# Performance work log

Measured on AMD Instinct MI355X. Metric: run time of the kernel, lower is better.

The kernel has to match this reference:

```python
import jax, jax.numpy as jnp
import numpy as np

N = 100000   # nodes
E = 300000   # directed edges
D = 256      # emb_dim
G = 4000     # graphs
L = 5        # num_layer
F_IN = 40    # num_atom_features
NUM_BOND_TYPE = 6       # pretrain-gnns convention; self-loop bond type = 4
NUM_BOND_DIRECTION = 3
EPS = 1e-5


def setup_inputs() -> dict:
    key = jax.random.key(0)
    ks = jax.random.split(key, 32)
    s = 0.05
    inp = {}
    inp["x"] = jax.random.normal(ks[0], (N, F_IN), jnp.float32)
    inp["edge_index"] = jax.random.randint(ks[1], (2, E), 0, N)
    inp["edge_attr"] = jax.random.randint(ks[2], (E, 2), 0, 3)
    inp["batch"] = jnp.sort(jax.random.randint(ks[3], (N,), 0, G))
    # atom embedding (Linear + ReLU)
    inp["embW"] = jax.random.normal(ks[4], (F_IN, D), jnp.float32) * s
    inp["embB"] = jnp.zeros((D,), jnp.float32)
    # per-layer GINConv params (stacked over layers)
    inp["ee1"] = jax.random.normal(ks[5], (L, NUM_BOND_TYPE, D), jnp.float32) * s
    inp["ee2"] = jax.random.normal(ks[6], (L, NUM_BOND_DIRECTION, D), jnp.float32) * s
    inp["W1"] = jax.random.normal(ks[7], (L, D, 2 * D), jnp.float32) * s
    inp["b1"] = jnp.zeros((L, 2 * D), jnp.float32)
    inp["W2"] = jax.random.normal(ks[8], (L, 2 * D, D), jnp.float32) * s
    inp["b2"] = jnp.zeros((L, D), jnp.float32)
    inp["bn_g"] = jnp.ones((L, D), jnp.float32)
    inp["bn_b"] = jnp.zeros((L, D), jnp.float32)
    # MLP head: 256 -> 256 -> 128 -> 64 -> 32 -> 1
    dims = [D, D, D // 2, D // 4, D // 8]
    kk = jax.random.split(ks[9], 5)
    for i in range(4):
        inp[f"hW{i}"] = jax.random.normal(kk[i], (dims[i], dims[i + 1]), jnp.float32) * s
        inp[f"hb{i}"] = jnp.zeros((dims[i + 1],), jnp.float32)
    inp["hWo"] = jax.random.normal(kk[4], (dims[4], 1), jnp.float32) * s
    inp["hbo"] = jnp.zeros((1,), jnp.float32)
    return inp


def reference(x, edge_index, edge_attr, batch, embW, embB, ee1, ee2, W1, b1, W2, b2,
              bn_g, bn_b, hW0, hb0, hW1, hb1, hW2, hb2, hW3, hb3, hWo, hbo):
    src, dst = edge_index[0], edge_index[1]
    ea0, ea1 = edge_attr[:, 0], edge_attr[:, 1]
    # x_embedding1: Linear + ReLU
    h = jax.nn.relu(x @ embW + embB)
    for l in range(L):
        # GINConv: gather source features + edge embeddings, scatter-add to dst
        msg = h[src] + ee1[l][ea0] + ee2[l][ea1]        # [E, D]
        agg = jax.ops.segment_sum(msg, dst, num_segments=N)
        # self-loop message (bond type 4, direction 0)
        agg = agg + h + ee1[l][4] + ee2[l][0]
        # GIN MLP: Linear(D, 2D) -> ReLU -> Linear(2D, D)
        h2 = jax.nn.relu(agg @ W1[l] + b1[l]) @ W2[l] + b2[l]
        # BatchNorm1d (training-mode batch statistics, biased variance)
        mu = h2.mean(axis=0)
        var = h2.var(axis=0)
        h2 = (h2 - mu) * jax.lax.rsqrt(var + EPS) * bn_g[l] + bn_b[l]
        if l < L - 1:
            h2 = jax.nn.relu(h2)
        # dropout with drop_ratio=0.0 -> identity
        h = h2
    # JK == 'last'
    node_rep = h
    # global_mean_pool
    counts = jnp.maximum(jax.ops.segment_sum(jnp.ones((N,), node_rep.dtype), batch, num_segments=G), 1.0)
    mol = jax.ops.segment_sum(node_rep, batch, num_segments=G) / counts[:, None]
    # MLP head
    z = jax.nn.relu(mol @ hW0 + hb0)
    z = jax.nn.relu(z @ hW1 + hb1)
    z = jax.nn.relu(z @ hW2 + hb2)
    z = jax.nn.relu(z @ hW3 + hb3)
    out = z @ hWo + hbo
    return out.reshape(-1)  # MolEmbed.view(-1), num_tasks == 1
```

## Files before the change

kernel.cpp:

```cpp
#include <hip/hip_runtime.h>
#include <hip/hip_bf16.h>

#define NN 100000
#define EE 300000
#define GG 4000
#define LL 5
#define GPB 4
#define SC_CHUNK 1024
#define SC_NB ((NN + SC_CHUNK - 1) / SC_CHUNK)

typedef _Float16 half8  __attribute__((ext_vector_type(8)));
typedef _Float16 half4v __attribute__((ext_vector_type(4)));
typedef float    f32x4  __attribute__((ext_vector_type(4)));

__device__ inline short f2h(float f) {
    _Float16 h = (_Float16)f;
    short s; __builtin_memcpy(&s, &h, 2); return s;
}

__device__ inline void async_load16(const void* g, void* l) {
    __builtin_amdgcn_global_load_lds(
        (const __attribute__((address_space(1))) unsigned int*)g,
        (__attribute__((address_space(3))) unsigned int*)l, 16, 0, 0);
}

__global__ __launch_bounds__(256) void k_count(
    int* __restrict__ deg, const int* __restrict__ ei)
{
    int e = blockIdx.x * 256 + threadIdx.x;
    if (e < EE) atomicAdd(&deg[ei[EE + e]], 1);
}

__global__ __launch_bounds__(256) void k_scan_partial(
    int* __restrict__ partial, const int* __restrict__ deg)
{
    int b = blockIdx.x, t = threadIdx.x;
    int lane = t & 63, w = t >> 6;
    int base = b * SC_CHUNK + t * 4;
    int s = 0;
#pragma unroll
    for (int j = 0; j < 4; ++j) {
        int i = base + j;
        if (i < NN) s += deg[i];
    }
#pragma unroll
    for (int off = 1; off < 64; off <<= 1) s += __shfl_xor(s, off, 64);
    __shared__ int ws[4];
    if (lane == 0) ws[w] = s;
    __syncthreads();
    if (t == 0) partial[b] = ws[0] + ws[1] + ws[2] + ws[3];
}

__global__ __launch_bounds__(128) void k_scan_base(
    int* __restrict__ bases, int* __restrict__ offs, const int* __restrict__ partial)
{
    int t = threadIdx.x;
    int lane = t & 63, w = t >> 6;
    int p = (t < SC_NB) ? partial[t] : 0;
    int x = p;
#pragma unroll
    for (int off = 1; off < 64; off <<= 1) {
        int nb = __shfl_up(x, off, 64);
        if (lane >= off) x += nb;
    }
    __shared__ int w0tot;
    if (t == 63) w0tot = x;
    __syncthreads();
    if (w == 1) x += w0tot;
    if (t < SC_NB) bases[t] = x - p;
    if (t == 0) offs[NN] = EE;
}

__global__ __launch_bounds__(256) void k_scan_final(
    int* __restrict__ offs, int* __restrict__ cursor,
    const int* __restrict__ deg, const int* __restrict__ bases)
{
    int b = blockIdx.x, t = threadIdx.x;
    int lane = t & 63, w = t >> 6;
    int base = b * SC_CHUNK + t * 4;
    int v[4], pre[4], run = 0;
#pragma unroll
    for (int j = 0; j < 4; ++j) {
        int i = base + j;
        v[j] = (i < NN) ? deg[i] : 0;
        pre[j] = run;
        run += v[j];
    }
    int x = run;
#pragma unroll
    for (int off = 1; off < 64; off <<= 1) {
        int nb = __shfl_up(x, off, 64);
        if (lane >= off) x += nb;
    }
    int tex = x - run;
    __shared__ int ws[4];
    if (lane == 63) ws[w] = x;
    __syncthreads();
    int woff = 0;
    for (int k = 0; k < 4; ++k) if (k < w) woff += ws[k];
    int tbase = bases[b] + woff + tex;
#pragma unroll
    for (int j = 0; j < 4; ++j) {
        int i = base + j;
        if (i < NN) { offs[i] = tbase + pre[j]; cursor[i] = tbase + pre[j]; }
    }
}

__global__ __launch_bounds__(256) void k_fill(
    int* __restrict__ csr, int* __restrict__ cursor,
    const int* __restrict__ ei, const int* __restrict__ ea)
{
    int e = blockIdx.x * 256 + threadIdx.x;
    if (e >= EE) return;
    int s = ei[e];
    int d = ei[EE + e];
    int c = ea[2 * e] * 3 + ea[2 * e + 1];
    int slot = atomicAdd(&cursor[d], 1);
    csr[slot] = s | (c << 20);
}

__device__ __forceinline__ void pack_body(
    short* __restrict__ dst, const float* __restrict__ src, int K, int Nsz,
    int nb, int kb, int l, int t, float (*T)[65])
{
    const float* s = src + ((size_t)l * K + kb * 32) * Nsz + nb * 64;
#pragma unroll
    for (int i = 0; i < 8; ++i) {
        int idx = i * 256 + t;
        int kk = idx >> 6, nl = idx & 63;
        T[kk][nl] = s[(size_t)kk * Nsz + nl];
    }
    __syncthreads();
    int nl = t >> 2, kq = t & 3;
    union { short s[8]; int4 v; } o;
#pragma unroll
    for (int j = 0; j < 8; ++j) o.s[j] = f2h(T[kq * 8 + j][nl]);
    short* d = dst + (((size_t)l * (K / 32) + kb) * Nsz + nb * 64 + nl) * 32 + kq * 8;
    *(int4*)d = o.v;
}

__global__ __launch_bounds__(256) void k_prologue(
    int* __restrict__ goffs, const int* __restrict__ batch,
    float* __restrict__ tbl, const float* __restrict__ ee1, const float* __restrict__ ee2,
    short* __restrict__ W1p, const float* __restrict__ W1,
    short* __restrict__ W2p, const float* __restrict__ W2,
    _Float16* __restrict__ Wep, const float* __restrict__ embW,
    int* __restrict__ deg, float* __restrict__ stats)
{
    __shared__ float T[32][65];
    int b = blockIdx.x, t = threadIdx.x;
    if (b < 391) {
        int n = b * 256 + t;
        if (n >= NN) return;
        int bb = batch[n];
        int bp = (n == 0) ? -1 : batch[n - 1];
        for (int g = bp + 1; g <= bb; ++g) goffs[g] = n;
        if (n == NN - 1)
            for (int g = bb + 1; g <= GG; ++g) goffs[g] = NN;
    } else if (b < 441) {
        int idx = b - 391;
        int c = idx % 10, l = idx / 10;
        int i1 = (c < 9) ? c / 3 : 4;
        int i2 = (c < 9) ? c % 3 : 0;
        tbl[((size_t)l * 10 + c) * 256 + t] =
            ee1[((size_t)l * 6 + i1) * 256 + t] + ee2[((size_t)l * 3 + i2) * 256 + t];
    } else if (b < 761) {
        int idx = b - 441;
        pack_body(W1p, W1, 256, 512, idx & 7, (idx >> 3) & 7, idx >> 6, t, T);
    } else if (b < 1081) {
        int idx = b - 761;
        pack_body(W2p, W2, 512, 256, idx & 3, (idx >> 2) & 15, idx >> 6, t, T);
    } else if (b < 1145) {
        int idx = (b - 1081) * 256 + t;
        int ks = idx >> 13, r = idx & 8191;
        int n = r >> 5, kk = r & 31;
        int k = ks * 32 + kk;
        float v = (k < 40) ? embW[(size_t)k * 256 + n] : 0.f;
        Wep[idx] = (_Float16)v;
    } else if (b < 1536) {
        int n = (b - 1145) * 256 + t;
        if (n < NN) deg[n] = 0;
    } else {
        int gi = (b - 1536) * 1024 + t * 4;
        float4 z = {0.f, 0.f, 0.f, 0.f};
        *(float4*)(stats + gi) = z;
    }
}

__global__ __launch_bounds__(256) void k_embed_mfma(
    _Float16* __restrict__ H, const float* __restrict__ x,
    const _Float16* __restrict__ Wep, const float* __restrict__ bias)
{
    __shared__ __align__(16) char smem[67584];
    _Float16* As = (_Float16*)smem;
    _Float16* Bs = (_Float16*)(smem + 16384);
    _Float16* Cs = (_Float16*)smem;

    const int t = threadIdx.x;
    const int w = t >> 6, lane = t & 63;
    const int quad = lane >> 4, l16 = lane & 15;
    const int wr = w >> 1, wc = w & 1;
    const int gm0 = blockIdx.x * 128;

#pragma unroll
    for (int i = 0; i < 8; ++i) {
        int u = i * 256 + t;
        async_load16((const char*)Wep + u * 16, (char*)Bs + u * 16);
    }

    {
        int row = t >> 1, half = t & 1;
        int rg = gm0 + row; if (rg > NN - 1) rg = NN - 1;
        const float* xp = x + (size_t)rg * 40 + half * 20;
        float v[20];
#pragma unroll
        for (int j = 0; j < 5; ++j) {
            float4 q = *(const float4*)(xp + j * 4);
            v[j * 4 + 0] = q.x; v[j * 4 + 1] = q.y; v[j * 4 + 2] = q.z; v[j * 4 + 3] = q.w;
        }
#pragma unroll
        for (int j = 0; j < 20; ++j) {
            int col = half * 20 + j;
            int ks = col >> 5, kk = col & 31;
            As[ks * 4096 + row * 32 + kk] = (_Float16)v[j];
        }
        int kb = 8 + half * 12;
#pragma unroll
        for (int j = 0; j < 12; ++j)
            As[4096 + row * 32 + kb + j] = (_Float16)0.f;
    }

    float biasreg[8];
#pragma unroll
    for (int nt = 0; nt < 8; ++nt)
        biasreg[nt] = bias[wc * 128 + nt * 16 + l16];

    f32x4 acc[4][8];
#pragma unroll
    for (int i = 0; i < 4; ++i)
#pragma unroll
        for (int j = 0; j < 8; ++j) acc[i][j] = (f32x4){0.f, 0.f, 0.f, 0.f};

    __syncthreads();

#pragma unroll
    for (int ks = 0; ks < 2; ++ks) {
        half8 af[4], bfr[8];
#pragma unroll
        for (int mt = 0; mt < 4; ++mt)
            af[mt] = *(const half8*)(As + ks * 4096 + (wr * 64 + mt * 16 + l16) * 32 + quad * 8);
#pragma unroll
        for (int nt = 0; nt < 8; ++nt)
            bfr[nt] = *(const half8*)(Bs + ks * 8192 + (wc * 128 + nt * 16 + l16) * 32 + quad * 8);
#pragma unroll
        for (int mt = 0; mt < 4; ++mt)
#pragma unroll
            for (int nt = 0; nt < 8; ++nt)
                acc[mt][nt] = __builtin_amdgcn_mfma_f32_16x16x32_f16(
                    af[mt], bfr[nt], acc[mt][nt], 0, 0, 0);
    }

    __syncthreads();
#pragma unroll
    for (int mt = 0; mt < 4; ++mt)
#pragma unroll
        for (int nt = 0; nt < 8; ++nt)
#pragma unroll
            for (int r = 0; r < 4; ++r) {
                int row = wr * 64 + mt * 16 + quad * 4 + r;
                int col = wc * 128 + nt * 16 + l16;
                Cs[row * 264 + col] = (_Float16)fmaxf(acc[mt][nt][r] + biasreg[nt], 0.f);
            }
    __syncthreads();
#pragma unroll
    for (int i = 0; i < 16; ++i) {
        int u = i * 256 + t;
        int m = u >> 5, ch = u & 31;
        int grow = gm0 + m;
        if (grow < NN)
            *(int4*)(H + (size_t)grow * 256 + ch * 8) =
                *(const int4*)(Cs + m * 264 + ch * 8);
    }
}

template <int AFF>
__global__ __launch_bounds__(256) void k_aggregate(
    _Float16* __restrict__ agg, const _Float16* __restrict__ hin,
    const int* __restrict__ offs, const int* __restrict__ csr,
    const float* __restrict__ tbl,
    const float* __restrict__ scale, const float* __restrict__ shift)
{
    int t = threadIdx.x;
    int w = t >> 6, lane = t & 63;
    int half = lane >> 5, l32 = lane & 31;
    int n = blockIdx.x * 8 + w * 2 + half;
    int ci = l32 * 2;

    const f32x4* tb4 = (const f32x4*)tbl;

    f32x4 sc0, sc1, sh0, sh1;
    if (AFF) {
        sc0 = ((const f32x4*)scale)[ci];  sc1 = ((const f32x4*)scale)[ci + 1];
        sh0 = ((const f32x4*)shift)[ci];  sh1 = ((const f32x4*)shift)[ci + 1];
    }

    half8 hv = *(const half8*)(hin + (size_t)n * 256 + l32 * 8);
    f32x4 a0 = tb4[9 * 64 + ci];
    f32x4 a1 = tb4[9 * 64 + ci + 1];
#pragma unroll
    for (int q = 0; q < 4; ++q) {
        float v0 = (float)hv[q];
        float v1 = (float)hv[4 + q];
        if (AFF) { v0 = fmaf(v0, sc0[q], sh0[q]); v1 = fmaf(v1, sc1[q], sh1[q]); }
        a0[q] += fmaxf(v0, 0.f);
        a1[q] += fmaxf(v1, 0.f);
    }

    int o0 = offs[n], o1 = offs[n + 1];
    for (int e = o0; e < o1; ++e) {
        int entry = csr[e];
        int s = entry & 0xFFFFF;
        int c = entry >> 20;
        half8 gv = *(const half8*)(hin + (size_t)s * 256 + l32 * 8);
        f32x4 t0 = tb4[c * 64 + ci];
        f32x4 t1 = tb4[c * 64 + ci + 1];
#pragma unroll
        for (int q = 0; q < 4; ++q) {
            float v0 = (float)gv[q];
            float v1 = (float)gv[4 + q];
            if (AFF) { v0 = fmaf(v0, sc0[q], sh0[q]); v1 = fmaf(v1, sc1[q], sh1[q]); }
            a0[q] += fmaxf(v0, 0.f) + t0[q];
            a1[q] += fmaxf(v1, 0.f) + t1[q];
        }
    }

    half8 o;
#pragma unroll
    for (int q = 0; q < 4; ++q) {
        o[q]     = (_Float16)a0[q];
        o[4 + q] = (_Float16)a1[q];
    }
    *(half8*)(agg + (size_t)n * 256 + l32 * 8) = o;
}

__global__ __launch_bounds__(256, 3) void k_fused_mlp(
    _Float16* __restrict__ H2, const _Float16* __restrict__ A,
    const short* __restrict__ W1p, const float* __restrict__ b1,
    const short* __restrict__ W2p, const float* __restrict__ b2,
    float* __restrict__ stats)
{
    __shared__ __align__(16) char smem[40960];
    _Float16* As = (_Float16*)smem;
    _Float16* Us = (_Float16*)(smem + 32768);
    _Float16* Cs = (_Float16*)smem;

    const int t = threadIdx.x;
    const int w = t >> 6, lane = t & 63;
    const int quad = lane >> 4, l16 = lane & 15;
    const int bm = blockIdx.x;
    const int gm0 = bm * 64;
    const int swz = l16 & 7;

#pragma unroll
    for (int i = 0; i < 8; ++i) {
        int u = i * 256 + t;
        int row = u >> 5;
        int gcol = (u & 31) ^ (row & 7);
        int grow = gm0 + row; if (grow > NN - 1) grow = NN - 1;
        async_load16(A + (size_t)grow * 256 + gcol * 8, (char*)As + u * 16);
    }

    const _Float16* w1w = (const _Float16*)W1p + ((size_t)(w * 16 + l16)) * 32 + quad * 8;
    const _Float16* w2w = (const _Float16*)W2p + ((size_t)(w * 64 + l16)) * 32 + quad * 8;

    half8 w1buf[8];
#pragma unroll
    for (int i = 0; i < 8; ++i)
        w1buf[i] = *(const half8*)(w1w + ((size_t)i * 512) * 32);
    half8 w2k0[4];
#pragma unroll
    for (int nt = 0; nt < 4; ++nt)
        w2k0[nt] = *(const half8*)(w2w + ((size_t)nt * 16) * 32);

    f32x4 acc2[4][4];
#pragma unroll
    for (int i = 0; i < 4; ++i)
#pragma unroll
        for (int j = 0; j < 4; ++j) acc2[i][j] = (f32x4){0.f, 0.f, 0.f, 0.f};

    __syncthreads();

    for (int j = 0; j < 8; ++j) {
        f32x4 acc1[4];
#pragma unroll
        for (int b = 0; b < 4; ++b) acc1[b] = (f32x4){0.f, 0.f, 0.f, 0.f};

#pragma unroll
        for (int kb = 0; kb < 8; ++kb) {
            int slotA = (kb * 4 + quad) ^ swz;
            half8 b1f[4];
#pragma unroll
            for (int urt = 0; urt < 4; ++urt)
                b1f[urt] = *(const half8*)(As + (urt * 16 + l16) * 256 + slotA * 8);
#pragma unroll
            for (int urt = 0; urt < 4; ++urt)
                acc1[urt] = __builtin_amdgcn_mfma_f32_16x16x32_f16(
                    w1buf[kb], b1f[urt], acc1[urt], 0, 0, 0);
        }

        half8 a2n[4];
#pragma unroll
        for (int nt = 0; nt < 4; ++nt)
            a2n[nt] = *(const half8*)(w2w + ((size_t)(j * 2 + 1) * 256 + nt * 16) * 32);

        {
            int ucl = w * 16 + quad * 4;
            float4 bv = *(const float4*)(b1 + j * 64 + ucl);
            int G = ucl >> 3;
            int hs = quad & 1;
#pragma unroll
            for (int urt = 0; urt < 4; ++urt) {
                int ur = urt * 16 + l16;
                int S = G ^ (ur & 7);
                half4v o;
                o[0] = (_Float16)fmaxf(acc1[urt][0] + bv.x, 0.f);
                o[1] = (_Float16)fmaxf(acc1[urt][1] + bv.y, 0.f);
                o[2] = (_Float16)fmaxf(acc1[urt][2] + bv.z, 0.f);
                o[3] = (_Float16)fmaxf(acc1[urt][3] + bv.w, 0.f);
                *(half4v*)(Us + ur * 64 + S * 8 + hs * 4) = o;
            }
        }
        asm volatile("s_waitcnt lgkmcnt(0)" ::: "memory");
        __builtin_amdgcn_s_barrier();
        __builtin_amdgcn_sched_barrier(0);

        if (j < 7) {
#pragma unroll
            for (int i = 0; i < 8; ++i)
                w1buf[i] = *(const half8*)(w1w + ((size_t)i * 512 + (j + 1) * 64) * 32);
        }

        {
            int slotU = quad ^ swz;
            half8 b2f[4];
#pragma unroll
            for (int mt = 0; mt < 4; ++mt)
                b2f[mt] = *(const half8*)(Us + (mt * 16 + l16) * 64 + slotU * 8);
#pragma unroll
            for (int nt = 0; nt < 4; ++nt)
#pragma unroll
                for (int mt = 0; mt < 4; ++mt)
                    acc2[nt][mt] = __builtin_amdgcn_mfma_f32_16x16x32_f16(
                        w2k0[nt], b2f[mt], acc2[nt][mt], 0, 0, 0);
        }
        if (j < 7) {
#pragma unroll
            for (int nt = 0; nt < 4; ++nt)
                w2k0[nt] = *(const half8*)(w2w + ((size_t)(j + 1) * 2 * 256 + nt * 16) * 32);
        }
        {
            int slotU = (4 + quad) ^ swz;
            half8 b2f[4];
#pragma unroll
            for (int mt = 0; mt < 4; ++mt)
                b2f[mt] = *(const half8*)(Us + (mt * 16 + l16) * 64 + slotU * 8);
#pragma unroll
            for (int nt = 0; nt < 4; ++nt)
#pragma unroll
                for (int mt = 0; mt < 4; ++mt)
                    acc2[nt][mt] = __builtin_amdgcn_mfma_f32_16x16x32_f16(
                        a2n[nt], b2f[mt], acc2[nt][mt], 0, 0, 0);
        }
        asm volatile("s_waitcnt lgkmcnt(0)" ::: "memory");
        __builtin_amdgcn_s_barrier();
        __builtin_amdgcn_sched_barrier(0);
    }

    int slot2 = bm & 63;
#pragma unroll
    for (int nt = 0; nt < 4; ++nt) {
        int nb = w * 64 + nt * 16 + quad * 4;
        float4 bv = *(const float4*)(b2 + nb);
        float s1[4] = {0.f, 0.f, 0.f, 0.f};
        float s2[4] = {0.f, 0.f, 0.f, 0.f};
#pragma unroll
        for (int mt = 0; mt < 4; ++mt) {
            int mr = mt * 16 + l16;
            int m = gm0 + mr;
            float v0 = acc2[nt][mt][0] + bv.x;
            float v1 = acc2[nt][mt][1] + bv.y;
            float v2 = acc2[nt][mt][2] + bv.z;
            float v3 = acc2[nt][mt][3] + bv.w;
            half4v o;
            o[0] = (_Float16)v0; o[1] = (_Float16)v1;
            o[2] = (_Float16)v2; o[3] = (_Float16)v3;
            *(half4v*)(Cs + mr * 264 + nb) = o;
            if (m < NN) {
                s1[0] += v0; s1[1] += v1; s1[2] += v2; s1[3] += v3;
                s2[0] += v0 * v0; s2[1] += v1 * v1;
                s2[2] += v2 * v2; s2[3] += v3 * v3;
            }
        }
#pragma unroll
        for (int r = 0; r < 4; ++r) {
            s1[r] += __shfl_xor(s1[r], 1, 64); s2[r] += __shfl_xor(s2[r], 1, 64);
            s1[r] += __shfl_xor(s1[r], 2, 64); s2[r] += __shfl_xor(s2[r], 2, 64);
            s1[r] += __shfl_xor(s1[r], 4, 64); s2[r] += __shfl_xor(s2[r], 4, 64);
            s1[r] += __shfl_xor(s1[r], 8, 64); s2[r] += __shfl_xor(s2[r], 8, 64);
            if (l16 == 0) {
                atomicAdd(&stats[slot2 * 512 + nb + r], s1[r]);
                atomicAdd(&stats[slot2 * 512 + 256 + nb + r], s2[r]);
            }
        }
    }
    __syncthreads();
#pragma unroll
    for (int i = 0; i < 8; ++i) {
        int u = i * 256 + t;
        int m = u >> 5, ch = u & 31;
        int grow = gm0 + m;
        if (grow < NN)
            *(int4*)(H2 + (size_t)grow * 256 + ch * 8) =
                *(const int4*)(Cs + m * 264 + ch * 8);
    }
}

__global__ __launch_bounds__(256) void k_bn_finalize(
    float* __restrict__ scale, float* __restrict__ shift,
    float* __restrict__ stats,
    const float* __restrict__ bn_g, const float* __restrict__ bn_b)
{
    int t = threadIdx.x;
    float s1 = 0.f, s2 = 0.f;
    for (int j = 0; j < 64; ++j) {
        s1 += stats[j * 512 + t];
        s2 += stats[j * 512 + 256 + t];
        stats[j * 512 + t] = 0.f;
        stats[j * 512 + 256 + t] = 0.f;
    }
    float mu  = s1 / (float)NN;
    float var = s2 / (float)NN - mu * mu;
    float sc  = bn_g[t] * rsqrtf(var + 1e-5f);
    scale[t] = sc;
    shift[t] = bn_b[t] - mu * sc;
}

__global__ __launch_bounds__(256) void k_pool(
    float* __restrict__ mol, const _Float16* __restrict__ h,
    const int* __restrict__ goffs,
    const float* __restrict__ scale, const float* __restrict__ shift)
{
    int g = blockIdx.x;
    int t = threadIdx.x;
    int s = goffs[g], e = goffs[g + 1];
    float sum = 0.f;
    for (int n = s; n < e; ++n) sum += (float)h[(size_t)n * 256 + t];
    int c = e - s; if (c < 1) c = 1;
    mol[(size_t)g * 256 + t] = fmaf(sum / (float)c, scale[t], shift[t]);
}

__global__ __launch_bounds__(256) void k_head(
    float* __restrict__ out, const float* __restrict__ mol,
    const float* __restrict__ hW0, const float* __restrict__ hb0,
    const float* __restrict__ hW1, const float* __restrict__ hb1,
    const float* __restrict__ hW2, const float* __restrict__ hb2,
    const float* __restrict__ hW3, const float* __restrict__ hb3,
    const float* __restrict__ hWo, const float* __restrict__ hbo)
{
    __shared__ float za[GPB][256];
    __shared__ float zb[GPB][256];
    const int t = threadIdx.x;
    const int g0 = blockIdx.x * GPB;

#pragma unroll
    for (int g = 0; g < GPB; ++g)
        za[g][t] = mol[(size_t)(g0 + g) * 256 + t];
    __syncthreads();

    {
        float acc[GPB];
#pragma unroll
        for (int g = 0; g < GPB; ++g) acc[g] = 0.f;
        for (int k = 0; k < 256; ++k) {
            float w = hW0[k * 256 + t];
#pragma unroll
            for (int g = 0; g < GPB; ++g) acc[g] = fmaf(za[g][k], w, acc[g]);
        }
        float b = hb0[t];
#pragma unroll
        for (int g = 0; g < GPB; ++g) zb[g][t] = fmaxf(acc[g] + b, 0.f);
    }
    __syncthreads();

    if (t < 128) {
        float acc[GPB];
#pragma unroll
        for (int g = 0; g < GPB; ++g) acc[g] = 0.f;
        for (int k = 0; k < 256; ++k) {
            float w = hW1[k * 128 + t];
#pragma unroll
            for (int g = 0; g < GPB; ++g) acc[g] = fmaf(zb[g][k], w, acc[g]);
        }
        float b = hb1[t];
#pragma unroll
        for (int g = 0; g < GPB; ++g) za[g][t] = fmaxf(acc[g] + b, 0.f);
    }
    __syncthreads();

    if (t < 64) {
        float acc[GPB];
#pragma unroll
        for (int g = 0; g < GPB; ++g) acc[g] = 0.f;
        for (int k = 0; k < 128; ++k) {
            float w = hW2[k * 64 + t];
#pragma unroll
            for (int g = 0; g < GPB; ++g) acc[g] = fmaf(za[g][k], w, acc[g]);
        }
        float b = hb2[t];
#pragma unroll
        for (int g = 0; g < GPB; ++g) zb[g][t] = fmaxf(acc[g] + b, 0.f);
    }
    __syncthreads();

    if (t < 32) {
        float acc[GPB];
#pragma unroll
        for (int g = 0; g < GPB; ++g) acc[g] = 0.f;
        for (int k = 0; k < 64; ++k) {
            float w = hW3[k * 32 + t];
#pragma unroll
            for (int g = 0; g < GPB; ++g) acc[g] = fmaf(zb[g][k], w, acc[g]);
        }
        float b = hb3[t];
#pragma unroll
        for (int g = 0; g < GPB; ++g) za[g][t] = fmaxf(acc[g] + b, 0.f);
    }
    __syncthreads();

    if (t < GPB) {
        float s = hbo[0];
        for (int k = 0; k < 32; ++k) s = fmaf(za[t][k], hWo[k], s);
        out[g0 + t] = s;
    }
}

extern "C" void kernel_launch(void* const* d_in, const int* in_sizes, int n_in,
                              void* d_out, int out_size, void* d_ws, size_t ws_size,
                              hipStream_t stream)
{
    const float* x    = (const float*)d_in[0];
    const int*   ei   = (const int*)d_in[1];
    const int*   ea   = (const int*)d_in[2];
    const int*   batch= (const int*)d_in[3];
    const float* embW = (const float*)d_in[4];
    const float* embB = (const float*)d_in[5];
    const float* ee1  = (const float*)d_in[6];
    const float* ee2  = (const float*)d_in[7];
    const float* W1   = (const float*)d_in[8];
    const float* b1   = (const float*)d_in[9];
    const float* W2   = (const float*)d_in[10];
    const float* b2   = (const float*)d_in[11];
    const float* bng  = (const float*)d_in[12];
    const float* bnb  = (const float*)d_in[13];
    const float* hW0  = (const float*)d_in[14];
    const float* hb0  = (const float*)d_in[15];
    const float* hW1  = (const float*)d_in[16];
    const float* hb1  = (const float*)d_in[17];
    const float* hW2  = (const float*)d_in[18];
    const float* hb2  = (const float*)d_in[19];
    const float* hW3  = (const float*)d_in[20];
    const float* hb3  = (const float*)d_in[21];
    const float* hWo  = (const float*)d_in[22];
    const float* hbo  = (const float*)d_in[23];
    float* out = (float*)d_out;

    char* ws = (char*)d_ws;
    size_t off = 0;
    _Float16* h2buf = (_Float16*)(ws + off); off += (size_t)NN * 256 * 2;
    _Float16* aggbuf= (_Float16*)(ws + off); off += (size_t)NN * 256 * 2;
    short* W1p      = (short*)(ws + off);    off += (size_t)5 * 131072 * 2;
    short* W2p      = (short*)(ws + off);    off += (size_t)5 * 131072 * 2;
    _Float16* Wep   = (_Float16*)(ws + off); off += (size_t)2 * 8192 * 2;
    float* tbl      = (float*)(ws + off);    off += (size_t)5 * 10 * 256 * 4;
    float* stats    = (float*)(ws + off);    off += (size_t)64 * 512 * 4;
    float* scale    = (float*)(ws + off);    off += 256 * 4;
    float* shift    = (float*)(ws + off);    off += 256 * 4;
    float* mol      = (float*)(ws + off);    off += (size_t)GG * 256 * 4;
    int* deg        = (int*)(ws + off);      off += (size_t)NN * 4;
    int* offs       = (int*)(ws + off);      off += (size_t)(NN + 1) * 4;
    int* cursor     = (int*)(ws + off);      off += (size_t)NN * 4;
    int* csr        = (int*)(ws + off);      off += (size_t)EE * 4;
    int* goffs      = (int*)(ws + off);      off += (size_t)(GG + 1) * 4;
    int* partial    = (int*)(ws + off);      off += 128 * 4;
    int* bases      = (int*)(ws + off);      off += 128 * 4;

    k_prologue<<<1568, 256, 0, stream>>>(goffs, batch, tbl, ee1, ee2,
                                         W1p, W1, W2p, W2, Wep, embW,
                                         deg, stats);
    k_count<<<(EE + 255) / 256, 256, 0, stream>>>(deg, ei);
    k_scan_partial<<<SC_NB, 256, 0, stream>>>(partial, deg);
    k_scan_base<<<1, 128, 0, stream>>>(bases, offs, partial);
    k_scan_final<<<SC_NB, 256, 0, stream>>>(offs, cursor, deg, bases);
    k_fill<<<(EE + 255) / 256, 256, 0, stream>>>(csr, cursor, ei, ea);

    k_embed_mfma<<<782, 256, 0, stream>>>(h2buf, x, Wep, embB);

    const int FB = (NN + 63) / 64;
    for (int l = 0; l < LL; ++l) {
        if (l == 0)
            k_aggregate<0><<<NN / 8, 256, 0, stream>>>(aggbuf, h2buf, offs, csr,
                                                       tbl, scale, shift);
        else
            k_aggregate<1><<<NN / 8, 256, 0, stream>>>(aggbuf, h2buf, offs, csr,
                                                       tbl + (size_t)l * 10 * 256, scale, shift);
        k_fused_mlp<<<FB, 256, 0, stream>>>(h2buf, aggbuf,
                                            W1p + (size_t)l * 131072, b1 + l * 512,
                                            W2p + (size_t)l * 131072, b2 + l * 256, stats);
        k_bn_finalize<<<1, 256, 0, stream>>>(scale, shift, stats, bng + l * 256, bnb + l * 256);
    }

    k_pool<<<GG, 256, 0, stream>>>(mol, h2buf, goffs, scale, shift);
    k_head<<<GG / GPB, 256, 0, stream>>>(out, mol,
                                         hW0, hb0, hW1, hb1, hW2, hb2, hW3, hb3, hWo, hbo);
}
```

Before: 900.5 us.

## Widen fused MLP hidden chunk to 128 and double-buffer W1 fragments

The fused GIN MLP kernel now processes the hidden dimension in 4 chunks of 128 instead of 8 chunks of 64. Each wave computes two 16-column tiles of the first GEMM per chunk, so the number of barrier pairs per block halves. W1 fragments are no longer held as eight registers per chunk; they are streamed through a two-slot register double buffer that is refilled during the inner K loop, and W2 loads are interleaved with the second-GEMM MFMAs. The intermediate LDS buffer doubles, raising shared memory to 48KB per block, which may limit occupancy under the 3-blocks-per-SM launch bound.

```diff
diff --git a/kernel.cpp b/kernel.cpp
--- a/kernel.cpp
+++ b/kernel.cpp
@@ -349,7 +349,7 @@
     const short* __restrict__ W2p, const float* __restrict__ b2,
     float* __restrict__ stats)
 {
-    __shared__ __align__(16) char smem[40960];
+    __shared__ __align__(16) char smem[49152];
     _Float16* As = (_Float16*)smem;
     _Float16* Us = (_Float16*)(smem + 32768);
     _Float16* Cs = (_Float16*)smem;
@@ -370,13 +370,15 @@
         async_load16(A + (size_t)grow * 256 + gcol * 8, (char*)As + u * 16);
     }
 
-    const _Float16* w1w = (const _Float16*)W1p + ((size_t)(w * 16 + l16)) * 32 + quad * 8;
+    const _Float16* w1w = (const _Float16*)W1p + ((size_t)(w * 32 + l16)) * 32 + quad * 8;
     const _Float16* w2w = (const _Float16*)W2p + ((size_t)(w * 64 + l16)) * 32 + quad * 8;
 
-    half8 w1buf[8];
-#pragma unroll
-    for (int i = 0; i < 8; ++i)
-        w1buf[i] = *(const half8*)(w1w + ((size_t)i * 512) * 32);
+    half8 a1d[2][2];
+#pragma unroll
+    for (int p = 0; p < 2; ++p)
+#pragma unroll
+        for (int ct = 0; ct < 2; ++ct)
+            a1d[p][ct] = *(const half8*)(w1w + ((size_t)p * 512 + ct * 16) * 32);
     half8 w2k0[4];
 #pragma unroll
     for (int nt = 0; nt < 4; ++nt)
@@ -386,17 +388,21 @@
 #pragma unroll
     for (int i = 0; i < 4; ++i)
 #pragma unroll
-        for (int j = 0; j < 4; ++j) acc2[i][j] = (f32x4){0.f, 0.f, 0.f, 0.f};
-
-    __syncthreads();
-
-    for (int j = 0; j < 8; ++j) {
-        f32x4 acc1[4];
-#pragma unroll
-        for (int b = 0; b < 4; ++b) acc1[b] = (f32x4){0.f, 0.f, 0.f, 0.f};
+        for (int jj = 0; jj < 4; ++jj) acc2[i][jj] = (f32x4){0.f, 0.f, 0.f, 0.f};
+
+    __syncthreads();
+
+    for (int j = 0; j < 4; ++j) {
+        f32x4 acc1[2][4];
+#pragma unroll
+        for (int a = 0; a < 2; ++a)
+#pragma unroll
+            for (int b = 0; b < 4; ++b) acc1[a][b] = (f32x4){0.f, 0.f, 0.f, 0.f};
 
 #pragma unroll
         for (int kb = 0; kb < 8; ++kb) {
+            half8 a1c0 = a1d[kb & 1][0];
+            half8 a1c1 = a1d[kb & 1][1];
             int slotA = (kb * 4 + quad) ^ swz;
             half8 b1f[4];
 #pragma unroll
@@ -404,18 +410,29 @@
                 b1f[urt] = *(const half8*)(As + (urt * 16 + l16) * 256 + slotA * 8);
 #pragma unroll
             for (int urt = 0; urt < 4; ++urt)
-                acc1[urt] = __builtin_amdgcn_mfma_f32_16x16x32_f16(
-                    w1buf[kb], b1f[urt], acc1[urt], 0, 0, 0);
-        }
-
-        half8 a2n[4];
+                acc1[0][urt] = __builtin_amdgcn_mfma_f32_16x16x32_f16(
+                    a1c0, b1f[urt], acc1[0][urt], 0, 0, 0);
+#pragma unroll
+            for (int urt = 0; urt < 4; ++urt)
+                acc1[1][urt] = __builtin_amdgcn_mfma_f32_16x16x32_f16(
+                    a1c1, b1f[urt], acc1[1][urt], 0, 0, 0);
+            if (kb < 6) {
+#pragma unroll
+                for (int ct = 0; ct < 2; ++ct)
+                    a1d[kb & 1][ct] = *(const half8*)(w1w +
+                        ((size_t)(kb + 2) * 512 + j * 128 + ct * 16) * 32);
+            }
+        }
+
+        half8 a2p[4];
 #pragma unroll
         for (int nt = 0; nt < 4; ++nt)
-            a2n[nt] = *(const half8*)(w2w + ((size_t)(j * 2 + 1) * 256 + nt * 16) * 32);
-
-        {
-            int ucl = w * 16 + quad * 4;
-            float4 bv = *(const float4*)(b1 + j * 64 + ucl);
+            a2p[nt] = *(const half8*)(w2w + ((size_t)(j * 4 + 1) * 256 + nt * 16) * 32);
+
+#pragma unroll
+        for (int ct = 0; ct < 2; ++ct) {
+            int ucl = w * 32 + ct * 16 + quad * 4;
+            float4 bv = *(const float4*)(b1 + j * 128 + ucl);
             int G = ucl >> 3;
             int hs = quad & 1;
 #pragma unroll
@@ -423,53 +440,90 @@
                 int ur = urt * 16 + l16;
                 int S = G ^ (ur & 7);
                 half4v o;
-                o[0] = (_Float16)fmaxf(acc1[urt][0] + bv.x, 0.f);
-                o[1] = (_Float16)fmaxf(acc1[urt][1] + bv.y, 0.f);
-                o[2] = (_Float16)fmaxf(acc1[urt][2] + bv.z, 0.f);
-                o[3] = (_Float16)fmaxf(acc1[urt][3] + bv.w, 0.f);
-                *(half4v*)(Us + ur * 64 + S * 8 + hs * 4) = o;
+                o[0] = (_Float16)fmaxf(acc1[ct][urt][0] + bv.x, 0.f);
+                o[1] = (_Float16)fmaxf(acc1[ct][urt][1] + bv.y, 0.f);
+                o[2] = (_Float16)fmaxf(acc1[ct][urt][2] + bv.z, 0.f);
+                o[3] = (_Float16)fmaxf(acc1[ct][urt][3] + bv.w, 0.f);
+                *(half4v*)(Us + ur * 128 + S * 8 + hs * 4) = o;
             }
         }
         asm volatile("s_waitcnt lgkmcnt(0)" ::: "memory");
         __builtin_amdgcn_s_barrier();
         __builtin_amdgcn_sched_barrier(0);
 
-        if (j < 7) {
-#pragma unroll
-            for (int i = 0; i < 8; ++i)
-                w1buf[i] = *(const half8*)(w1w + ((size_t)i * 512 + (j + 1) * 64) * 32);
-        }
-
         {
             int slotU = quad ^ swz;
             half8 b2f[4];
 #pragma unroll
             for (int mt = 0; mt < 4; ++mt)
-                b2f[mt] = *(const half8*)(Us + (mt * 16 + l16) * 64 + slotU * 8);
+                b2f[mt] = *(const half8*)(Us + (mt * 16 + l16) * 128 + slotU * 8);
 #pragma unroll
             for (int nt = 0; nt < 4; ++nt)
 #pragma unroll
                 for (int mt = 0; mt < 4; ++mt)
                     acc2[nt][mt] = __builtin_amdgcn_mfma_f32_16x16x32_f16(
                         w2k0[nt], b2f[mt], acc2[nt][mt], 0, 0, 0);
-        }
-        if (j < 7) {
 #pragma unroll
             for (int nt = 0; nt < 4; ++nt)
-                w2k0[nt] = *(const half8*)(w2w + ((size_t)(j + 1) * 2 * 256 + nt * 16) * 32);
+                w2k0[nt] = *(const half8*)(w2w + ((size_t)(j * 4 + 2) * 256 + nt * 16) * 32);
         }
         {
             int slotU = (4 + quad) ^ swz;
             half8 b2f[4];
 #pragma unroll
             for (int mt = 0; mt < 4; ++mt)
-                b2f[mt] = *(const half8*)(Us + (mt * 16 + l16) * 64 + slotU * 8);
+                b2f[mt] = *(const half8*)(Us + (mt * 16 + l16) * 128 + slotU * 8);
 #pragma unroll
             for (int nt = 0; nt < 4; ++nt)
 #pragma unroll
                 for (int mt = 0; mt < 4; ++mt)
                     acc2[nt][mt] = __builtin_amdgcn_mfma_f32_16x16x32_f16(
-                        a2n[nt], b2f[mt], acc2[nt][mt], 0, 0, 0);
+                        a2p[nt], b2f[mt], acc2[nt][mt], 0, 0, 0);
+#pragma unroll
+            for (int nt = 0; nt < 4; ++nt)
+                a2p[nt] = *(const half8*)(w2w + ((size_t)(j * 4 + 3) * 256 + nt * 16) * 32);
+            if (j < 3) {
+#pragma unroll
+                for (int ct = 0; ct < 2; ++ct)
+                    a1d[0][ct] = *(const half8*)(w1w +
+                        ((size_t)(j + 1) * 128 + ct * 16) * 32);
+            }
+        }
+        {
+            int slotU = (8 + quad) ^ swz;
+            half8 b2f[4];
+#pragma unroll
+            for (int mt = 0; mt < 4; ++mt)
+                b2f[mt] = *(const half8*)(Us + (mt * 16 + l16) * 128 + slotU * 8);
+#pragma unroll
+            for (int nt = 0; nt < 4; ++nt)
+#pragma unroll
+                for (int mt = 0; mt < 4; ++mt)
+                    acc2[nt][mt] = __builtin_amdgcn_mfma_f32_16x16x32_f16(
+                        w2k0[nt], b2f[mt], acc2[nt][mt], 0, 0, 0);
+            if (j < 3) {
+#pragma unroll
+                for (int nt = 0; nt < 4; ++nt)
+                    w2k0[nt] = *(const half8*)(w2w +
+                        ((size_t)(j + 1) * 4 * 256 + nt * 16) * 32);
+#pragma unroll
+                for (int ct = 0; ct < 2; ++ct)
+                    a1d[1][ct] = *(const half8*)(w1w +
+                        ((size_t)(1 * 512) + (j + 1) * 128 + ct * 16) * 32);
+            }
+        }
+        {
+            int slotU = (12 + quad) ^ swz;
+            half8 b2f[4];
+#pragma unroll
+            for (int mt = 0; mt < 4; ++mt)
+                b2f[mt] = *(const half8*)(Us + (mt * 16 + l16) * 128 + slotU * 8);
+#pragma unroll
+            for (int nt = 0; nt < 4; ++nt)
+#pragma unroll
+                for (int mt = 0; mt < 4; ++mt)
+                    acc2[nt][mt] = __builtin_amdgcn_mfma_f32_16x16x32_f16(
+                        a2p[nt], b2f[mt], acc2[nt][mt], 0, 0, 0);
         }
         asm volatile("s_waitcnt lgkmcnt(0)" ::: "memory");
         __builtin_amdgcn_s_barrier();
```

After: 960.3 us. +6.6%, slower.
